# Optimization experiments

Hardware: AMD Instinct MI355X
Metric: run time of the kernel (lower is better)

Reference implementation:

```python
import jax, jax.numpy as jnp
import numpy as np

B, C, H, W = 4, 96, 224, 224
WS, NH = 7, 3
HID = 384
N = WS * WS  # tokens per window
HD = C // NH

def _make_rel_index():
    coords = np.stack(np.meshgrid(np.arange(WS), np.arange(WS), indexing='ij')).reshape(2, -1)
    rel = (coords[:, :, None] - coords[:, None, :]).transpose(1, 2, 0)  # (N,N,2)
    rel[:, :, 0] += WS - 1
    rel[:, :, 1] += WS - 1
    rel[:, :, 0] *= 2 * WS - 1
    return jnp.asarray(rel.sum(-1), dtype=jnp.int32)  # (N,N) in [0, 169)

def setup_inputs() -> dict:
    key = jax.random.key(0)
    ks = jax.random.split(key, 8)
    def w(k, shape):
        return jax.random.normal(k, shape, jnp.float32) * 0.02
    return {
        "x": jax.random.normal(ks[0], (B, C, H, W), jnp.float32),
        "norm1_g": jnp.ones((C,), jnp.float32),
        "norm1_b": jnp.zeros((C,), jnp.float32),
        "qkv_w": w(ks[1], (C, 3 * C)),
        "qkv_b": jnp.zeros((3 * C,), jnp.float32),
        "proj_w": w(ks[2], (C, C)),
        "proj_b": jnp.zeros((C,), jnp.float32),
        "rel_bias": w(ks[3], ((2 * WS - 1) ** 2, NH)),
        "norm2_g": jnp.ones((C,), jnp.float32),
        "norm2_b": jnp.zeros((C,), jnp.float32),
        "mlp_w1": w(ks[4], (C, HID)),
        "mlp_b1": jnp.zeros((HID,), jnp.float32),
        "mlp_w2": w(ks[5], (HID, C)),
        "mlp_b2": jnp.zeros((C,), jnp.float32),
        "rel_index": _make_rel_index(),
    }

def _layernorm(x, g, b, eps=1e-5):
    m = jnp.mean(x, axis=-1, keepdims=True)
    v = jnp.mean(jnp.square(x - m), axis=-1, keepdims=True)
    return (x - m) * jax.lax.rsqrt(v + eps) * g + b

def _window_partition(x):  # x: (B,H,W,C) -> (B*nW, N, C)
    xw = x.reshape(B, H // WS, WS, W // WS, WS, C)
    xw = xw.transpose(0, 1, 3, 2, 4, 5)
    return xw.reshape(-1, N, C)

def _window_reverse(xw):  # (B*nW, N, C) -> (B,H,W,C)
    x = xw.reshape(B, H // WS, W // WS, WS, WS, C)
    x = x.transpose(0, 1, 3, 2, 4, 5)
    return x.reshape(B, H, W, C)

def _window_attention(xw, qkv_w, qkv_b, proj_w, proj_b, rel_bias, rel_index):
    nW = xw.shape[0]
    qkv = (xw @ qkv_w + qkv_b).reshape(nW, N, 3, NH, HD)
    q, k, v = qkv[:, :, 0], qkv[:, :, 1], qkv[:, :, 2]  # (nW, N, NH, HD)
    scale = HD ** -0.5
    attn = jnp.einsum('wnhd,wmhd->whnm', q, k) * scale  # (nW, NH, N, N)
    bias = rel_bias[rel_index]                           # (N, N, NH)
    attn = attn + bias.transpose(2, 0, 1)[None]
    attn = jax.nn.softmax(attn, axis=-1)
    out = jnp.einsum('whnm,wmhd->wnhd', attn, v).reshape(nW, N, C)
    return out @ proj_w + proj_b

def reference(x, norm1_g, norm1_b, qkv_w, qkv_b, proj_w, proj_b, rel_bias,
              norm2_g, norm2_b, mlp_w1, mlp_b1, mlp_w2, mlp_b2, rel_index):
    # x: (B,C,H,W)
    shortcut = x
    xt = x.transpose(0, 2, 3, 1)  # (B,H,W,C)
    xt = _layernorm(xt, norm1_g, norm1_b)
    xw = _window_partition(xt)
    aw = _window_attention(xw, qkv_w, qkv_b, proj_w, proj_b, rel_bias, rel_index)
    a = _window_reverse(aw).transpose(0, 3, 1, 2)  # (B,C,H,W)
    x = shortcut + a
    shortcut2 = x
    xt = x.transpose(0, 2, 3, 1)
    xt = _layernorm(xt, norm2_g, norm2_b)
    h = jax.nn.gelu(xt @ mlp_w1 + mlp_b1, approximate=False)
    xt = h @ mlp_w2 + mlp_b2
    return shortcut2 + xt.transpose(0, 3, 1, 2)
```

## Files before the change

kernel.cpp:

```cpp
#include <hip/hip_runtime.h>
#include <hip/hip_bf16.h>
#include <cstdint>

#define HW 50176
#define CB 96
#define BATCH 4
#define NTOK (BATCH*HW)
#define NWIN 4096
#define HIDDEN 384

typedef __attribute__((ext_vector_type(8))) short bf16x8;
typedef __attribute__((ext_vector_type(4))) short bf16x4;
typedef __attribute__((ext_vector_type(4))) float f32x4;

#define MFMA32(a,b,c) __builtin_amdgcn_mfma_f32_16x16x32_bf16(a,b,c,0,0,0)

#if __has_builtin(__builtin_amdgcn_mfma_f32_16x16x16bf16_1k)
#define MFMA16(a,b,c) __builtin_amdgcn_mfma_f32_16x16x16bf16_1k(a,b,c,0,0,0)
#elif __has_builtin(__builtin_amdgcn_mfma_f32_16x16x16_bf16)
#define MFMA16(a,b,c) __builtin_amdgcn_mfma_f32_16x16x16_bf16(a,b,c,0,0,0)
#else
static __device__ inline f32x4 mfma16_asm(bf16x4 a, bf16x4 b, f32x4 c){
  asm volatile("v_mfma_f32_16x16x16_bf16 %0, %1, %2, %0" : "+v"(c) : "v"(a), "v"(b));
  return c;
}
#define MFMA16(a,b,c) mfma16_asm(a,b,c)
#endif

#if __has_builtin(__builtin_amdgcn_rcpf)
#define FRCP(x) __builtin_amdgcn_rcpf(x)
#else
#define FRCP(x) (1.f/(x))
#endif
#if __has_builtin(__builtin_amdgcn_exp2f)
#define FEXP2(x) __builtin_amdgcn_exp2f(x)
#else
#define FEXP2(x) exp2f(x)
#endif

__device__ inline unsigned short f2bf(float f){
  union { float f; unsigned u; } x; x.f = f;
  unsigned r = x.u + 0x7fffu + ((x.u >> 16) & 1u);
  return (unsigned short)(r >> 16);
}
__device__ inline float bf2f(unsigned short h){
  union { unsigned u; float f; } x; x.u = ((unsigned)h) << 16; return x.f;
}
__device__ inline unsigned pack2(float a, float b){
  return (unsigned)f2bf(a) | ((unsigned)f2bf(b) << 16);
}

__device__ inline float gelu_tanh(float v){
  float t  = v * v;
  float t2 = fmaf(0.044715f, t, 1.f);
  float u  = v * t2;
  float e  = FEXP2(u * 2.302344536f);
  float r  = FRCP(e + 1.f);
  return fmaf(-v, r, v);
}

__global__ __launch_bounds__(256) void prep_all(
    const float* __restrict__ qkv_w, const float* __restrict__ proj_w,
    const float* __restrict__ w1, const float* __restrict__ w2,
    const float* __restrict__ rb, const int* __restrict__ ri,
    unsigned short* __restrict__ qkvT, unsigned short* __restrict__ projT,
    unsigned short* __restrict__ w1P, unsigned short* __restrict__ w2P,
    float* __restrict__ biasT){
  int b = blockIdx.x;
  if (b < 108){
    int id = b * 256 + threadIdx.x;
    int n = id / 96, k = id - n * 96;
    qkvT[id] = f2bf(qkv_w[k * 288 + n]);
  } else if (b < 144){
    int id = (b - 108) * 256 + threadIdx.x;
    int n = id / 96, k = id - n * 96;
    projT[id] = f2bf(proj_w[k * 96 + n]);
  } else if (b < 288){
    int t = (b - 144) * 256 + threadIdx.x;
    int e = t & 7, lane = (t >> 3) & 63, rest = t >> 9;
    int ks = rest % 3, n = rest / 3;
    int k = ks * 32 + (lane >> 4) * 8 + e;
    int o = n * 16 + (lane & 15);
    w1P[t] = f2bf(w1[k * HIDDEN + o]);
  } else if (b < 432){
    int t = (b - 288) * 256 + threadIdx.x;
    int e = t & 3, l = (t >> 2) & 63, rest = t >> 8;
    int n = rest % 24, co = rest / 24;
    int k = 16 * n + 4 * (l >> 4) + e;
    int c = 16 * co + (l & 15);
    w2P[t] = f2bf(w2[k * CB + c]);
  } else {
    int t = (b - 432) * 256 + threadIdx.x;
    int h = t >> 12, k = (t >> 6) & 63, q = t & 63;
    float v = 0.f;
    if (k < 49 && q < 49) v = rb[ri[q * 49 + k] * 3 + h];
    biasT[((h * 16 + (k >> 2)) * 64 + q) * 4 + (k & 3)] = v;
  }
}

__global__ __launch_bounds__(256) void ln_first(const float* __restrict__ x,
    const float* __restrict__ g, const float* __restrict__ bta,
    unsigned short* __restrict__ out){
  __shared__ float s[64][97];
  int tid = threadIdx.x;
  int blk = blockIdx.x;
  int bi = blk / (HW / 64);
  int pos0 = (blk - bi * (HW / 64)) * 64;
  const float* xb = x + (size_t)bi * CB * HW + pos0;
  for (int it = 0; it < 24; ++it){
    int idx = it * 256 + tid;
    int c = idx >> 6, p = idx & 63;
    s[p][c] = xb[(size_t)c * HW + p];
  }
  __syncthreads();
  int p = tid >> 2, part = tid & 3;
  float sum = 0.f, sq = 0.f;
  #pragma unroll
  for (int j = 0; j < 24; ++j){ float v = s[p][part * 24 + j]; sum += v; sq += v * v; }
  sum += __shfl_xor(sum, 1); sq += __shfl_xor(sq, 1);
  sum += __shfl_xor(sum, 2); sq += __shfl_xor(sq, 2);
  float mean = sum * (1.f / 96.f);
  float var  = sq * (1.f / 96.f) - mean * mean;
  float rs = rsqrtf(var + 1e-5f);
  size_t tok = (size_t)bi * HW + pos0 + p;
  float vv[24];
  #pragma unroll
  for (int j = 0; j < 24; ++j){
    int c = part * 24 + j;
    vv[j] = (s[p][c] - mean) * rs * g[c] + bta[c];
  }
  unsigned pw[12];
  #pragma unroll
  for (int j = 0; j < 12; ++j) pw[j] = pack2(vv[2 * j], vv[2 * j + 1]);
  uint4* dst = (uint4*)(out + tok * CB + part * 24);
  dst[0] = make_uint4(pw[0], pw[1], pw[2], pw[3]);
  dst[1] = make_uint4(pw[4], pw[5], pw[6], pw[7]);
  dst[2] = make_uint4(pw[8], pw[9], pw[10], pw[11]);
}

__global__ __launch_bounds__(256) void attn_fused(
    unsigned short* __restrict__ xn,
    const unsigned short* __restrict__ qkvT,
    const float* __restrict__ qkv_b,
    const float* __restrict__ biasT){
  __shared__ unsigned short sQ[64][104];
  __shared__ unsigned short sK[64][104];
  __shared__ unsigned short sVT[3][32][72];
  __shared__ unsigned short sP[64][72];
  int tid = threadIdx.x;
  int wid = blockIdx.x;
  int bi = wid >> 10;
  int wy = (wid & 1023) >> 5, wx = wid & 31;
  int rowbase = bi * HW + (wy * 7) * 224 + wx * 7;

  int wv = tid >> 6, lane = tid & 63;
  int r = lane & 15, g = lane >> 4;
  int kg = g * 8;
  int nbase = (wv < 2) ? wv * 5 : 10 + (wv - 2) * 4;
  int ncnt  = (wv < 2) ? 5 : 4;
  int arow[4];
  #pragma unroll
  for (int m = 0; m < 4; ++m){
    int rr = m * 16 + r; if (rr > 48) rr = 48;
    arow[m] = rowbase + (rr / 7) * 224 + (rr % 7);
  }
  f32x4 acc[4][5];
  #pragma unroll
  for (int m = 0; m < 4; ++m)
    #pragma unroll
    for (int j = 0; j < 5; ++j) acc[m][j] = (f32x4){0.f,0.f,0.f,0.f};
  #pragma unroll
  for (int k0 = 0; k0 < 96; k0 += 32){
    bf16x8 a[4];
    #pragma unroll
    for (int m = 0; m < 4; ++m)
      a[m] = *(const bf16x8*)(xn + (size_t)arow[m] * CB + kg + k0);
    #pragma unroll
    for (int j = 0; j < 5; ++j){
      if (j < ncnt){
        int nt = nbase + j;
        bf16x8 b = *(const bf16x8*)(qkvT + (nt * 16 + r) * CB + kg + k0);
        #pragma unroll
        for (int m = 0; m < 4; ++m)
          acc[m][j] = MFMA32(a[m], b, acc[m][j]);
      }
    }
  }
  int orow = g * 4;
  #pragma unroll
  for (int j = 0; j < 5; ++j){
    if (j < ncnt){
      int nt = nbase + j;
      int col = nt * 16 + r;
      float bs = qkv_b[col];
      #pragma unroll
      for (int m = 0; m < 4; ++m){
        #pragma unroll
        for (int i = 0; i < 4; ++i){
          int row = m * 16 + orow + i;
          float v = (row < 49) ? acc[m][j][i] + bs : 0.f;
          if (col < 96)       sQ[row][col] = f2bf(v * 0.17677669529663687f);
          else if (col < 192) sK[row][col - 96] = f2bf(v);
          else { int cc = col - 192; sVT[cc >> 5][cc & 31][row] = f2bf(v); }
        }
      }
    }
  }
  __syncthreads();

  int qrow = 16 * wv + r;
  int qq = 16 * wv + 4 * g;
  #pragma unroll
  for (int h = 0; h < 3; ++h){
    bf16x8 bq = *(const bf16x8*)&sQ[qrow][h * 32 + kg];
    f32x4 sacc[4];
    #pragma unroll
    for (int j = 0; j < 4; ++j)
      sacc[j] = *(const f32x4*)&biasT[(((h * 16) + 4 * j + g) * 64 + qrow) * 4];
    #pragma unroll
    for (int j = 0; j < 4; ++j){
      bf16x8 ak = *(const bf16x8*)&sK[16 * j + r][h * 32 + kg];
      sacc[j] = MFMA32(ak, bq, sacc[j]);
    }
    float mx = -1e30f;
    #pragma unroll
    for (int j = 0; j < 4; ++j)
      #pragma unroll
      for (int i = 0; i < 4; ++i){
        int k = 16 * j + 4 * g + i;
        if (k <= 48) mx = fmaxf(mx, sacc[j][i]);
      }
    mx = fmaxf(mx, __shfl_xor(mx, 16));
    mx = fmaxf(mx, __shfl_xor(mx, 32));
    float p[4][4], sum = 0.f;
    #pragma unroll
    for (int j = 0; j < 4; ++j)
      #pragma unroll
      for (int i = 0; i < 4; ++i){
        int k = 16 * j + 4 * g + i;
        float pv = (k <= 48) ? __expf(sacc[j][i] - mx) : 0.f;
        p[j][i] = pv; sum += pv;
      }
    sum += __shfl_xor(sum, 16);
    sum += __shfl_xor(sum, 32);
    float inv = 1.f / sum;
    #pragma unroll
    for (int j = 0; j < 4; ++j){
      uint2 w2;
      w2.x = pack2(p[j][0] * inv, p[j][1] * inv);
      w2.y = pack2(p[j][2] * inv, p[j][3] * inv);
      *(uint2*)&sP[qrow][16 * j + 4 * g] = w2;
    }
    f32x4 oacc[2];
    oacc[0] = (f32x4){0.f,0.f,0.f,0.f};
    oacc[1] = (f32x4){0.f,0.f,0.f,0.f};
    #pragma unroll
    for (int k0 = 0; k0 < 64; k0 += 32){
      bf16x8 ap = *(const bf16x8*)&sP[16 * wv + r][k0 + kg];
      #pragma unroll
      for (int n = 0; n < 2; ++n){
        bf16x8 bv = *(const bf16x8*)&sVT[h][n * 16 + r][k0 + kg];
        oacc[n] = MFMA32(ap, bv, oacc[n]);
      }
    }
    #pragma unroll
    for (int i = 0; i < 4; ++i){
      int q = qq + i;
      if (q < 49){
        int tok = rowbase + (q / 7) * 224 + (q % 7);
        unsigned short* dst = xn + (size_t)tok * CB + h * 32 + r;
        dst[0]  = f2bf(oacc[0][i]);
        dst[16] = f2bf(oacc[1][i]);
      }
    }
  }
}

__global__ __launch_bounds__(256) void proj_ln2(
    unsigned short* __restrict__ att,
    const unsigned short* __restrict__ projT, const float* __restrict__ proj_b,
    const float* __restrict__ x, const float* __restrict__ gam,
    const float* __restrict__ bet,
    float* __restrict__ x2out){
  int tid = threadIdx.x, blk = blockIdx.x;
  int bi = blk / (HW / 64);
  int pos0 = (blk - bi * (HW / 64)) * 64;
  int wv = tid >> 6, lane = tid & 63, r = lane & 15, g = lane >> 4;
  int pos = pos0 + wv * 16 + r;
  size_t tok = (size_t)bi * HW + pos;

  bf16x8 ab[3];
  #pragma unroll
  for (int ks = 0; ks < 3; ++ks)
    ab[ks] = *(const bf16x8*)(att + tok * CB + ks * 32 + g * 8);
  f32x4 acc[6];
  #pragma unroll
  for (int co = 0; co < 6; ++co) acc[co] = (f32x4){0.f,0.f,0.f,0.f};
  #pragma unroll
  for (int ks = 0; ks < 3; ++ks){
    #pragma unroll
    for (int co = 0; co < 6; ++co){
      bf16x8 a = *(const bf16x8*)(projT + (co * 16 + r) * CB + ks * 32 + g * 8);
      acc[co] = MFMA32(a, ab[ks], acc[co]);
    }
  }
  const float* xb = x + (size_t)bi * CB * HW + pos;
  float* ob = x2out + (size_t)bi * CB * HW + pos;
  float y[24];
  float sum = 0.f, sq = 0.f;
  #pragma unroll
  for (int co = 0; co < 6; ++co){
    float4 bv = *(const float4*)&proj_b[co * 16 + 4 * g];
    float bb[4] = {bv.x, bv.y, bv.z, bv.w};
    #pragma unroll
    for (int i = 0; i < 4; ++i){
      int c = co * 16 + 4 * g + i;
      float v = acc[co][i] + bb[i] + xb[(size_t)c * HW];
      ob[(size_t)c * HW] = v;
      y[co * 4 + i] = v;
      sum += v; sq += v * v;
    }
  }
  sum += __shfl_xor(sum, 16); sq += __shfl_xor(sq, 16);
  sum += __shfl_xor(sum, 32); sq += __shfl_xor(sq, 32);
  float mean = sum * (1.f / 96.f);
  float var  = sq * (1.f / 96.f) - mean * mean;
  float rs = rsqrtf(var + 1e-5f);
  #pragma unroll
  for (int co = 0; co < 6; ++co){
    float4 gv = *(const float4*)&gam[co * 16 + 4 * g];
    float4 bv = *(const float4*)&bet[co * 16 + 4 * g];
    float gg[4] = {gv.x, gv.y, gv.z, gv.w};
    float bb[4] = {bv.x, bv.y, bv.z, bv.w};
    float o[4];
    #pragma unroll
    for (int i = 0; i < 4; ++i)
      o[i] = (y[co * 4 + i] - mean) * rs * gg[i] + bb[i];
    uint2 w2 = make_uint2(pack2(o[0], o[1]), pack2(o[2], o[3]));
    *(uint2*)(att + tok * CB + co * 16 + 4 * g) = w2;
  }
}

__global__ __launch_bounds__(512) void mlp_fused(
    const unsigned short* __restrict__ xn2,
    const unsigned short* __restrict__ w1P,
    const unsigned short* __restrict__ w2P,
    const float* __restrict__ b1, const float* __restrict__ b2,
    float* __restrict__ io){
  __shared__ unsigned short sW[36864];
  int tid = threadIdx.x, blk = blockIdx.x;
  int bi = blk / (HW / 256);
  int pos0 = (blk - bi * (HW / 256)) * 256;
  #pragma unroll
  for (int it = 0; it < 9; ++it){
    int idx = it * 512 + tid;
    *(uint4*)&sW[idx * 8] = ((const uint4*)w1P)[idx];
  }
  __syncthreads();

  int wv = tid >> 6, lane = tid & 63, r = lane & 15, g = lane >> 4;
  int pos = pos0 + wv * 32 + r;
  size_t tok = (size_t)bi * HW + pos;

  bf16x8 xb[2][3];
  #pragma unroll
  for (int m = 0; m < 2; ++m)
    #pragma unroll
    for (int ks = 0; ks < 3; ++ks)
      xb[m][ks] = *(const bf16x8*)(xn2 + (tok + m * 16) * CB + ks * 32 + g * 8);

  f32x4 acc2[2][6];
  #pragma unroll
  for (int m = 0; m < 2; ++m)
    #pragma unroll
    for (int co = 0; co < 6; ++co) acc2[m][co] = (f32x4){0.f,0.f,0.f,0.f};

  #pragma unroll
  for (int n = 0; n < 24; ++n){
    f32x4 acc0 = (f32x4){0.f,0.f,0.f,0.f};
    f32x4 acc1 = (f32x4){0.f,0.f,0.f,0.f};
    #pragma unroll
    for (int ks = 0; ks < 3; ++ks){
      bf16x8 a = *(const bf16x8*)&sW[((n * 3 + ks) * 64 + lane) * 8];
      acc0 = MFMA32(a, xb[0][ks], acc0);
      acc1 = MFMA32(a, xb[1][ks], acc1);
    }
    float4 bv = *(const float4*)&b1[n * 16 + 4 * g];
    union { unsigned u[2]; bf16x4 v; } u0, u1;
    u0.u[0] = pack2(gelu_tanh(acc0[0] + bv.x), gelu_tanh(acc0[1] + bv.y));
    u0.u[1] = pack2(gelu_tanh(acc0[2] + bv.z), gelu_tanh(acc0[3] + bv.w));
    u1.u[0] = pack2(gelu_tanh(acc1[0] + bv.x), gelu_tanh(acc1[1] + bv.y));
    u1.u[1] = pack2(gelu_tanh(acc1[2] + bv.z), gelu_tanh(acc1[3] + bv.w));
    bf16x4 h0 = u0.v, h1 = u1.v;
    #pragma unroll
    for (int co = 0; co < 6; ++co){
      bf16x4 a2 = *(const bf16x4*)(w2P + ((co * 24 + n) * 64 + lane) * 4);
      acc2[0][co] = MFMA16(a2, h0, acc2[0][co]);
      acc2[1][co] = MFMA16(a2, h1, acc2[1][co]);
    }
  }
  #pragma unroll
  for (int co = 0; co < 6; ++co){
    float4 bv = *(const float4*)&b2[co * 16 + 4 * g];
    float bb[4] = {bv.x, bv.y, bv.z, bv.w};
    #pragma unroll
    for (int i = 0; i < 4; ++i){
      int c = co * 16 + 4 * g + i;
      float* p0 = io + ((size_t)bi * CB + c) * HW + pos;
      #pragma unroll
      for (int m = 0; m < 2; ++m)
        p0[m * 16] = p0[m * 16] + acc2[m][co][i] + bb[i];
    }
  }
}

extern "C" void kernel_launch(void* const* d_in, const int* in_sizes, int n_in,
                              void* d_out, int out_size, void* d_ws, size_t ws_size,
                              hipStream_t stream){
  const float* x        = (const float*)d_in[0];
  const float* n1g      = (const float*)d_in[1];
  const float* n1b      = (const float*)d_in[2];
  const float* qkv_w    = (const float*)d_in[3];
  const float* qkv_b    = (const float*)d_in[4];
  const float* proj_w   = (const float*)d_in[5];
  const float* proj_b   = (const float*)d_in[6];
  const float* rel_bias = (const float*)d_in[7];
  const float* n2g      = (const float*)d_in[8];
  const float* n2b      = (const float*)d_in[9];
  const float* w1       = (const float*)d_in[10];
  const float* b1       = (const float*)d_in[11];
  const float* w2       = (const float*)d_in[12];
  const float* b2       = (const float*)d_in[13];
  const int* rel_index  = (const int*)d_in[14];
  float* outp = (float*)d_out;

  char* ws = (char*)d_ws;
  unsigned short* qkvT  = (unsigned short*)ws;
  unsigned short* projT = qkvT + 288 * 96;
  unsigned short* w1P   = projT + 96 * 96;
  unsigned short* w2P   = w1P + 36864;
  float* biasT          = (float*)(ws + 221184);
  unsigned short* xn    = (unsigned short*)(ws + 221184 + 49152);

  prep_all<<<dim3(480), 256, 0, stream>>>(qkv_w, proj_w, w1, w2, rel_bias,
                                          rel_index, qkvT, projT, w1P, w2P, biasT);

  ln_first  <<<dim3(NTOK / 64), 256, 0, stream>>>(x, n1g, n1b, xn);
  attn_fused<<<dim3(NWIN),      256, 0, stream>>>(xn, qkvT, qkv_b, biasT);
  proj_ln2  <<<dim3(NTOK / 64), 256, 0, stream>>>(xn, projT, proj_b, x, n2g, n2b, outp);
  mlp_fused <<<dim3(NTOK / 256), 512, 0, stream>>>(xn, w1P, w2P, b1, b2, outp);
}
```

Before: 254.0 us.

## Move LN2 into MLP kernel, store residual as bf16, stage W2 in LDS

The projection kernel now writes only the bf16 residual sum x+attn and no longer writes the fp32 intermediate to the output buffer. The MLP kernel recomputes LayerNorm2 from that bf16 tensor, stages both W1 and W2 in shared memory (doubling LDS per block), and writes the final output as the bf16 residual plus the MLP result instead of a read-modify-write of fp32 output. This removes one fp32 write and read of the full activation tensor. The cost is lower residual precision, since the shortcut is rounded to bf16, and 144KB of LDS per block, which may cut occupancy. The residual reloads in the epilogue are strided 2-byte gathers.

```diff
diff --git a/kernel.cpp b/kernel.cpp
--- a/kernel.cpp
+++ b/kernel.cpp
@@ -276,12 +276,10 @@
   }
 }
 
-__global__ __launch_bounds__(256) void proj_ln2(
+__global__ __launch_bounds__(256) void proj_res(
     unsigned short* __restrict__ att,
     const unsigned short* __restrict__ projT, const float* __restrict__ proj_b,
-    const float* __restrict__ x, const float* __restrict__ gam,
-    const float* __restrict__ bet,
-    float* __restrict__ x2out){
+    const float* __restrict__ x){
   int tid = threadIdx.x, blk = blockIdx.x;
   int bi = blk / (HW / 64);
   int pos0 = (blk - bi * (HW / 64)) * 64;
@@ -305,56 +303,35 @@
     }
   }
   const float* xb = x + (size_t)bi * CB * HW + pos;
-  float* ob = x2out + (size_t)bi * CB * HW + pos;
-  float y[24];
-  float sum = 0.f, sq = 0.f;
   #pragma unroll
   for (int co = 0; co < 6; ++co){
     float4 bv = *(const float4*)&proj_b[co * 16 + 4 * g];
     float bb[4] = {bv.x, bv.y, bv.z, bv.w};
+    float y[4];
     #pragma unroll
     for (int i = 0; i < 4; ++i){
       int c = co * 16 + 4 * g + i;
-      float v = acc[co][i] + bb[i] + xb[(size_t)c * HW];
-      ob[(size_t)c * HW] = v;
-      y[co * 4 + i] = v;
-      sum += v; sq += v * v;
-    }
-  }
-  sum += __shfl_xor(sum, 16); sq += __shfl_xor(sq, 16);
-  sum += __shfl_xor(sum, 32); sq += __shfl_xor(sq, 32);
-  float mean = sum * (1.f / 96.f);
-  float var  = sq * (1.f / 96.f) - mean * mean;
-  float rs = rsqrtf(var + 1e-5f);
-  #pragma unroll
-  for (int co = 0; co < 6; ++co){
-    float4 gv = *(const float4*)&gam[co * 16 + 4 * g];
-    float4 bv = *(const float4*)&bet[co * 16 + 4 * g];
-    float gg[4] = {gv.x, gv.y, gv.z, gv.w};
-    float bb[4] = {bv.x, bv.y, bv.z, bv.w};
-    float o[4];
-    #pragma unroll
-    for (int i = 0; i < 4; ++i)
-      o[i] = (y[co * 4 + i] - mean) * rs * gg[i] + bb[i];
-    uint2 w2 = make_uint2(pack2(o[0], o[1]), pack2(o[2], o[3]));
+      y[i] = acc[co][i] + bb[i] + xb[(size_t)c * HW];
+    }
+    uint2 w2 = make_uint2(pack2(y[0], y[1]), pack2(y[2], y[3]));
     *(uint2*)(att + tok * CB + co * 16 + 4 * g) = w2;
   }
 }
 
 __global__ __launch_bounds__(512) void mlp_fused(
-    const unsigned short* __restrict__ xn2,
-    const unsigned short* __restrict__ w1P,
-    const unsigned short* __restrict__ w2P,
+    const unsigned short* __restrict__ x2b,
+    const unsigned short* __restrict__ wP,
     const float* __restrict__ b1, const float* __restrict__ b2,
+    const float* __restrict__ gam, const float* __restrict__ bet,
     float* __restrict__ io){
-  __shared__ unsigned short sW[36864];
+  __shared__ unsigned short sW[73728];
   int tid = threadIdx.x, blk = blockIdx.x;
   int bi = blk / (HW / 256);
   int pos0 = (blk - bi * (HW / 256)) * 256;
   #pragma unroll
-  for (int it = 0; it < 9; ++it){
+  for (int it = 0; it < 18; ++it){
     int idx = it * 512 + tid;
-    *(uint4*)&sW[idx * 8] = ((const uint4*)w1P)[idx];
+    *(uint4*)&sW[idx * 8] = ((const uint4*)wP)[idx];
   }
   __syncthreads();
 
@@ -364,10 +341,45 @@
 
   bf16x8 xb[2][3];
   #pragma unroll
-  for (int m = 0; m < 2; ++m)
-    #pragma unroll
-    for (int ks = 0; ks < 3; ++ks)
-      xb[m][ks] = *(const bf16x8*)(xn2 + (tok + m * 16) * CB + ks * 32 + g * 8);
+  for (int m = 0; m < 2; ++m){
+    bf16x8 xc[3];
+    float xv[24];
+    float sum = 0.f, sq = 0.f;
+    #pragma unroll
+    for (int ks = 0; ks < 3; ++ks){
+      xc[ks] = *(const bf16x8*)(x2b + (tok + m * 16) * CB + ks * 32 + g * 8);
+      #pragma unroll
+      for (int e = 0; e < 8; ++e){
+        float v = bf2f((unsigned short)xc[ks][e]);
+        xv[ks * 8 + e] = v;
+        sum += v; sq += v * v;
+      }
+    }
+    sum += __shfl_xor(sum, 16); sq += __shfl_xor(sq, 16);
+    sum += __shfl_xor(sum, 32); sq += __shfl_xor(sq, 32);
+    float mean = sum * (1.f / 96.f);
+    float var  = sq * (1.f / 96.f) - mean * mean;
+    float rs = rsqrtf(var + 1e-5f);
+    #pragma unroll
+    for (int ks = 0; ks < 3; ++ks){
+      float4 g0 = *(const float4*)&gam[ks * 32 + g * 8];
+      float4 g1 = *(const float4*)&gam[ks * 32 + g * 8 + 4];
+      float4 b0 = *(const float4*)&bet[ks * 32 + g * 8];
+      float4 b1v = *(const float4*)&bet[ks * 32 + g * 8 + 4];
+      float gg[8] = {g0.x,g0.y,g0.z,g0.w,g1.x,g1.y,g1.z,g1.w};
+      float bb[8] = {b0.x,b0.y,b0.z,b0.w,b1v.x,b1v.y,b1v.z,b1v.w};
+      unsigned pw[4];
+      #pragma unroll
+      for (int e2 = 0; e2 < 4; ++e2){
+        float v0 = (xv[ks * 8 + 2*e2]   - mean) * rs * gg[2*e2]   + bb[2*e2];
+        float v1 = (xv[ks * 8 + 2*e2+1] - mean) * rs * gg[2*e2+1] + bb[2*e2+1];
+        pw[e2] = pack2(v0, v1);
+      }
+      union { unsigned u[4]; bf16x8 v; } u;
+      u.u[0] = pw[0]; u.u[1] = pw[1]; u.u[2] = pw[2]; u.u[3] = pw[3];
+      xb[m][ks] = u.v;
+    }
+  }
 
   f32x4 acc2[2][6];
   #pragma unroll
@@ -394,7 +406,7 @@
     bf16x4 h0 = u0.v, h1 = u1.v;
     #pragma unroll
     for (int co = 0; co < 6; ++co){
-      bf16x4 a2 = *(const bf16x4*)(w2P + ((co * 24 + n) * 64 + lane) * 4);
+      bf16x4 a2 = *(const bf16x4*)&sW[36864 + ((co * 24 + n) * 64 + lane) * 4];
       acc2[0][co] = MFMA16(a2, h0, acc2[0][co]);
       acc2[1][co] = MFMA16(a2, h1, acc2[1][co]);
     }
@@ -408,8 +420,10 @@
       int c = co * 16 + 4 * g + i;
       float* p0 = io + ((size_t)bi * CB + c) * HW + pos;
       #pragma unroll
-      for (int m = 0; m < 2; ++m)
-        p0[m * 16] = p0[m * 16] + acc2[m][co][i] + bb[i];
+      for (int m = 0; m < 2; ++m){
+        float x2s = bf2f(x2b[(tok + m * 16) * CB + c]);
+        p0[m * 16] = x2s + acc2[m][co][i] + bb[i];
+      }
     }
   }
 }
@@ -447,6 +461,6 @@
 
   ln_first  <<<dim3(NTOK / 64), 256, 0, stream>>>(x, n1g, n1b, xn);
   attn_fused<<<dim3(NWIN),      256, 0, stream>>>(xn, qkvT, qkv_b, biasT);
-  proj_ln2  <<<dim3(NTOK / 64), 256, 0, stream>>>(xn, projT, proj_b, x, n2g, n2b, outp);
-  mlp_fused <<<dim3(NTOK / 256), 512, 0, stream>>>(xn, w1P, w2P, b1, b2, outp);
-}
+  proj_res  <<<dim3(NTOK / 64), 256, 0, stream>>>(xn, projT, proj_b, x);
+  mlp_fused <<<dim3(NTOK / 256), 512, 0, stream>>>(xn, w1P, b1, b2, n2g, n2b, outp);
+}
```

After: 232.5 us. -8.5%, faster.
